# Performance work log

Measured on AMD Instinct MI355X. Metric: run time of the kernel, lower is better.

## Reference

```python
import jax, jax.numpy as jnp
import numpy as np

NU, NI = 100000, 50000
N = NU + NI
CU, CI = 100, 100
D = 64
NL = 3
NNZ = 4_000_000
CNNZ = 5000
B = 4096


def setup_inputs() -> dict:
    key = jax.random.key(0)
    ks = jax.random.split(key, 24)
    def edges(k1, k2, k3, nnz, n):
        return (jax.random.randint(k1, (nnz,), 0, n, dtype=jnp.int32),
                jax.random.randint(k2, (nnz,), 0, n, dtype=jnp.int32),
                jax.random.uniform(k3, (nnz,), dtype=jnp.float32) * 0.05)
    ar, ac, av = edges(ks[0], ks[1], ks[2], NNZ, N)
    s1r, s1c, s1v = edges(ks[3], ks[4], ks[5], NNZ, N)
    s2r, s2c, s2v = edges(ks[6], ks[7], ks[8], NNZ, N)
    cr, cc, cv = edges(ks[9], ks[10], ks[11], CNNZ, CU + CI)
    return {
        "user_emb": jax.random.normal(ks[12], (NU, D), dtype=jnp.float32) * 0.1,
        "item_emb": jax.random.normal(ks[13], (NI, D), dtype=jnp.float32) * 0.1,
        "adj_rows": ar, "adj_cols": ac, "adj_vals": av,
        "sg1_rows": s1r, "sg1_cols": s1c, "sg1_vals": s1v,
        "sg2_rows": s2r, "sg2_cols": s2c, "sg2_vals": s2v,
        "uc": jax.random.uniform(ks[14], (NU, CU), dtype=jnp.float32),
        "ic": jax.random.uniform(ks[15], (NI, CI), dtype=jnp.float32),
        "cg_rows": cr, "cg_cols": cc, "cg_vals": cv,
        "users": jax.random.randint(ks[16], (B,), 0, NU, dtype=jnp.int32),
        "items": jax.random.randint(ks[17], (B,), 0, NI, dtype=jnp.int32),
        "neg_items": jax.random.randint(ks[18], (B,), 0, NI, dtype=jnp.int32),
    }


def _gcn(rows, cols, vals, ego, n):
    """n_layers of SpMM propagation + mean over layer outputs (incl. layer 0)."""
    acc = ego
    x = ego
    for _ in range(NL):
        x = jax.ops.segment_sum(vals[:, None] * x[cols], rows, num_segments=n)
        acc = acc + x
    return acc / (NL + 1)


def reference(user_emb, item_emb,
              adj_rows, adj_cols, adj_vals,
              sg1_rows, sg1_cols, sg1_vals,
              sg2_rows, sg2_cols, sg2_vals,
              uc, ic, cg_rows, cg_cols, cg_vals,
              users, items, neg_items):
    ego = jnp.concatenate([user_emb, item_emb], axis=0)  # [N, D]
    e0 = _gcn(adj_rows, adj_cols, adj_vals, ego, N)
    e1 = _gcn(sg1_rows, sg1_cols, sg1_vals, ego, N)
    e2 = _gcn(sg2_rows, sg2_cols, sg2_vals, ego, N)
    # community GCN: project node embeddings onto community space, propagate, lift back
    ucf = uc.T @ user_emb                                # [CU, D]
    icf = ic.T @ item_emb                                # [CI, D]
    ec = _gcn(cg_rows, cg_cols, cg_vals,
              jnp.concatenate([ucf, icf], axis=0), CU + CI)
    u3 = uc @ ec[:CU]                                    # [NU, D]
    i3 = ic @ ec[CU:]                                    # [NI, D]
    user_f = jnp.concatenate([e0[:NU], e1[:NU], e2[:NU], u3], axis=1)  # [NU, 4D]
    item_f = jnp.concatenate([e0[NU:], e1[NU:], e2[NU:], i3], axis=1)  # [NI, 4D]
    ue = user_f[users]
    ie = item_f[items]
    ne = item_f[neg_items]
    # sup_logits = <u, i_pos> - <u, i_neg>
    return jnp.sum(ue * (ie - ne), axis=-1)
```

## Files before the change

### kernel.cpp

```cpp
#include <hip/hip_runtime.h>
#include <hip/hip_fp16.h>
#include <cstdint>
#include <cstddef>

#define NU_ 100000
#define NI_ 50000
#define NN_ 150000
#define D_  64
#define NNZ_ 4000000
#define CN_ 200
#define CNNZ_ 5000
#define B_ 4096

#define NB2   128
#define RPB2  1172
#define SLICE 112
#define NBLK  512

#define PROJB 1024

#define SCALE_ 32.0f
#define INVS_  (1.0f / 32.0f)

typedef float v2f __attribute__((ext_vector_type(2)));

__device__ __forceinline__ float cv8(unsigned char b) {
    return __builtin_amdgcn_cvt_f32_fp8((int)b, 0);
}


__global__ __launch_bounds__(256) void k_tofp8(const float* __restrict__ a,
                                               const float* __restrict__ b,
                                               unsigned char* __restrict__ dst) {
    size_t off = ((size_t)blockIdx.x * 256 + threadIdx.x) * 4;
    if (off >= (size_t)NN_ * D_) return;
    const float* src = (off < (size_t)NU_ * D_) ? a + off : b + (off - (size_t)NU_ * D_);
    float4 f = *(const float4*)src;
    int p = 0;
    p = __builtin_amdgcn_cvt_pk_fp8_f32(f.x * SCALE_, f.y * SCALE_, p, false);
    p = __builtin_amdgcn_cvt_pk_fp8_f32(f.z * SCALE_, f.w * SCALE_, p, true);
    *(unsigned*)(dst + off) = (unsigned)p;
}

__global__ __launch_bounds__(256) void k_bin(const int* __restrict__ rows,
                                             const int* __restrict__ cols,
                                             const float* __restrict__ vals,
                                             int* __restrict__ bcnt,
                                             int2* __restrict__ gbuf) {
    __shared__ int lcur[NB2];
    int t = threadIdx.x;
    for (int i = t; i < NB2; i += 256) lcur[i] = 0;
    __syncthreads();
    size_t blockbase = (size_t)blockIdx.x * NB2 * SLICE;

    for (int base = blockIdx.x * 1024; base < NNZ_; base += gridDim.x * 1024) {
        int i0 = base + t * 4;
        if (i0 < NNZ_) {
            int4   r4 = *(const int4*)(rows + i0);
            int4   c4 = *(const int4*)(cols + i0);
            float4 v4 = *(const float4*)(vals + i0);
            #pragma unroll
            for (int k = 0; k < 4; k++) {
                int r = (k == 0) ? r4.x : (k == 1) ? r4.y : (k == 2) ? r4.z : r4.w;
                int c = (k == 0) ? c4.x : (k == 1) ? c4.y : (k == 2) ? c4.z : c4.w;
                float v = (k == 0) ? v4.x : (k == 1) ? v4.y : (k == 2) ? v4.z : v4.w;
                int b  = r / RPB2;
                int rl = r - b * RPB2;
                int pos = atomicAdd(&lcur[b], 1);
                if (pos < SLICE)
                    gbuf[blockbase + (size_t)b * SLICE + pos] =
                        make_int2((rl << 18) | c, __float_as_int(v));
            }
        }
    }
    __syncthreads();
    for (int i = t; i < NB2; i += 256)
        bcnt[(size_t)blockIdx.x * NB2 + i] = min(lcur[i], SLICE);
}


__global__ void k_btot(const int* __restrict__ bcnt, int* __restrict__ btot) {
    __shared__ int s[256];
    int b = blockIdx.x, t = threadIdx.x;
    int sum = 0;
    for (int sl = t; sl < NBLK; sl += 256) sum += bcnt[(size_t)sl * NB2 + b];
    s[t] = sum;
    __syncthreads();
    for (int o = 128; o > 0; o >>= 1) {
        if (t < o) s[t] += s[t + o];
        __syncthreads();
    }
    if (t == 0) btot[b] = s[0];
}

__global__ void k_bscan(const int* __restrict__ btot, int* __restrict__ bbase,
                        int* __restrict__ row_ptr) {
    __shared__ int s[NB2];
    int t = threadIdx.x;
    int v = btot[t];
    s[t] = v;
    __syncthreads();
    for (int o = 1; o < NB2; o <<= 1) {
        int x = (t >= o) ? s[t - o] : 0;
        __syncthreads();
        s[t] += x;
        __syncthreads();
    }
    bbase[t] = s[t] - v;
    if (t == NB2 - 1) row_ptr[NN_] = s[t];
}


__global__ __launch_bounds__(1024) void k_csr(const int* __restrict__ bcnt,
                                              const int2* __restrict__ gbuf,
                                              const int* __restrict__ bbase,
                                              int* __restrict__ row_ptr,
                                              int2* __restrict__ ep) {
    __shared__ int h[RPB2];
    __shared__ int hx[RPB2];
    __shared__ int aux[1024];
    int b = blockIdx.x, t = threadIdx.x;
    for (int i = t; i < RPB2; i += 1024) h[i] = 0;
    __syncthreads();

    int sl = t >> 1, part = t & 1;
    int n = bcnt[(size_t)sl * NB2 + b];
    const int2* src = gbuf + ((size_t)sl * NB2 + b) * SLICE;

    for (int i = part; i < n; i += 2) {
        int rl = ((unsigned)src[i].x) >> 18;
        atomicAdd(&h[rl], 1);
    }
    __syncthreads();

    int a0 = (2 * t     < RPB2) ? h[2 * t]     : 0;
    int a1 = (2 * t + 1 < RPB2) ? h[2 * t + 1] : 0;
    aux[t] = a0 + a1;
    __syncthreads();
    for (int o = 1; o < 1024; o <<= 1) {
        int x = (t >= o) ? aux[t - o] : 0;
        __syncthreads();
        aux[t] += x;
        __syncthreads();
    }
    int excl = t ? aux[t - 1] : 0;
    if (2 * t     < RPB2) hx[2 * t]     = excl;
    if (2 * t + 1 < RPB2) hx[2 * t + 1] = excl + a0;
    __syncthreads();

    int base = bbase[b];
    int r0 = b * RPB2;
    int rows_b = min(RPB2, NN_ - r0);
    for (int i = t; i < rows_b; i += 1024) row_ptr[r0 + i] = base + hx[i];
    __syncthreads();

    for (int i = part; i < n; i += 2) {
        int2 e = src[i];
        int rl = ((unsigned)e.x) >> 18;
        int c  = e.x & 0x3FFFF;
        int pos = base + atomicAdd(&hx[rl], 1);
        ep[pos] = make_int2(c, e.y);
    }
}


__global__ __launch_bounds__(256) void k_spmm(const int* __restrict__ rp,
                                              const int2* __restrict__ ep,
                                              const unsigned char* __restrict__ xq,
                                              unsigned char* __restrict__ xn) {
    int w = (blockIdx.x * 256 + threadIdx.x) >> 6;
    if (w >= NN_) return;
    int lane = threadIdx.x & 63;
    int oct = lane >> 3;
    int l8  = lane & 7;
    int j0 = rp[w], j1 = rp[w + 1];
    float a0 = 0.f, a1 = 0.f, a2 = 0.f, a3 = 0.f, a4 = 0.f, a5 = 0.f, a6 = 0.f, a7 = 0.f;
    #pragma unroll 2
    for (int j = j0; j < j1; j += 8) {
        int je = j + oct;
        int2 e = (je < j1) ? ep[je] : make_int2(0, 0);
        float v = __int_as_float(e.y);
        uint2 raw = *(const uint2*)(xq + (size_t)e.x * D_ + l8 * 8);
        v2f f01 = __builtin_amdgcn_cvt_pk_f32_fp8((int)raw.x, false);
        v2f f23 = __builtin_amdgcn_cvt_pk_f32_fp8((int)raw.x, true);
        v2f f45 = __builtin_amdgcn_cvt_pk_f32_fp8((int)raw.y, false);
        v2f f67 = __builtin_amdgcn_cvt_pk_f32_fp8((int)raw.y, true);
        a0 += v * f01[0]; a1 += v * f01[1]; a2 += v * f23[0]; a3 += v * f23[1];
        a4 += v * f45[0]; a5 += v * f45[1]; a6 += v * f67[0]; a7 += v * f67[1];
    }
    #pragma unroll
    for (int o = 32; o >= 8; o >>= 1) {
        a0 += __shfl_xor(a0, o, 64); a1 += __shfl_xor(a1, o, 64);
        a2 += __shfl_xor(a2, o, 64); a3 += __shfl_xor(a3, o, 64);
        a4 += __shfl_xor(a4, o, 64); a5 += __shfl_xor(a5, o, 64);
        a6 += __shfl_xor(a6, o, 64); a7 += __shfl_xor(a7, o, 64);
    }
    if (lane < 8) {
        int p0 = 0, p1 = 0;
        p0 = __builtin_amdgcn_cvt_pk_fp8_f32(a0, a1, p0, false);
        p0 = __builtin_amdgcn_cvt_pk_fp8_f32(a2, a3, p0, true);
        p1 = __builtin_amdgcn_cvt_pk_fp8_f32(a4, a5, p1, false);
        p1 = __builtin_amdgcn_cvt_pk_fp8_f32(a6, a7, p1, true);
        uint2 o2; o2.x = (unsigned)p0; o2.y = (unsigned)p1;
        *(uint2*)(xn + (size_t)w * D_ + l8 * 8) = o2;
    }
}


__global__ __launch_bounds__(256) void k_spmm_s(const int* __restrict__ rp,
                                                const int2* __restrict__ ep,
                                                const unsigned char* __restrict__ xq,
                                                const int* __restrict__ users,
                                                const int* __restrict__ items,
                                                const int* __restrict__ negs,
                                                float* __restrict__ x3s) {
    int s = (blockIdx.x * 256 + threadIdx.x) >> 6;
    if (s >= 3 * B_) return;
    int lane = threadIdx.x & 63;
    int oct = lane >> 3;
    int l8  = lane & 7;
    int node;
    if (s < B_)          node = users[s];
    else if (s < 2 * B_) node = NU_ + items[s - B_];
    else                 node = NU_ + negs[s - 2 * B_];
    int j0 = rp[node], j1 = rp[node + 1];
    float a0 = 0.f, a1 = 0.f, a2 = 0.f, a3 = 0.f, a4 = 0.f, a5 = 0.f, a6 = 0.f, a7 = 0.f;
    #pragma unroll 2
    for (int j = j0; j < j1; j += 8) {
        int je = j + oct;
        int2 e = (je < j1) ? ep[je] : make_int2(0, 0);
        float v = __int_as_float(e.y);
        uint2 raw = *(const uint2*)(xq + (size_t)e.x * D_ + l8 * 8);
        v2f f01 = __builtin_amdgcn_cvt_pk_f32_fp8((int)raw.x, false);
        v2f f23 = __builtin_amdgcn_cvt_pk_f32_fp8((int)raw.x, true);
        v2f f45 = __builtin_amdgcn_cvt_pk_f32_fp8((int)raw.y, false);
        v2f f67 = __builtin_amdgcn_cvt_pk_f32_fp8((int)raw.y, true);
        a0 += v * f01[0]; a1 += v * f01[1]; a2 += v * f23[0]; a3 += v * f23[1];
        a4 += v * f45[0]; a5 += v * f45[1]; a6 += v * f67[0]; a7 += v * f67[1];
    }
    #pragma unroll
    for (int o = 32; o >= 8; o >>= 1) {
        a0 += __shfl_xor(a0, o, 64); a1 += __shfl_xor(a1, o, 64);
        a2 += __shfl_xor(a2, o, 64); a3 += __shfl_xor(a3, o, 64);
        a4 += __shfl_xor(a4, o, 64); a5 += __shfl_xor(a5, o, 64);
        a6 += __shfl_xor(a6, o, 64); a7 += __shfl_xor(a7, o, 64);
    }
    if (lane < 8) {
        float* dst = x3s + (size_t)s * D_ + l8 * 8;
        *(float4*)dst       = make_float4(a0, a1, a2, a3);
        *(float4*)(dst + 4) = make_float4(a4, a5, a6, a7);
    }
}


template<bool FIRST>
__global__ void k_dot_graph(const float* __restrict__ ue, const float* __restrict__ ie,
                            const unsigned char* __restrict__ x1,
                            const unsigned char* __restrict__ x2,
                            const float* __restrict__ x3s,
                            const int* __restrict__ users, const int* __restrict__ items,
                            const int* __restrict__ negs, float* __restrict__ out) {
    int w = (blockIdx.x * blockDim.x + threadIdx.x) >> 6;
    int lane = threadIdx.x & 63;
    if (w >= B_) return;
    int u = users[w], ip = items[w], in_ = negs[w];
    size_t ou = (size_t)u * D_ + lane;
    size_t oi = (size_t)(NU_ + ip) * D_ + lane;
    size_t on = (size_t)(NU_ + in_) * D_ + lane;
    float du = ue[(size_t)u * D_ + lane]
             + (cv8(x1[ou]) + cv8(x2[ou]) + x3s[(size_t)w * D_ + lane]) * INVS_;
    float di = ie[(size_t)ip * D_ + lane]
             + (cv8(x1[oi]) + cv8(x2[oi]) + x3s[(size_t)(B_ + w) * D_ + lane]) * INVS_;
    float dn = ie[(size_t)in_ * D_ + lane]
             + (cv8(x1[on]) + cv8(x2[on]) + x3s[(size_t)(2 * B_ + w) * D_ + lane]) * INVS_;
    float p = du * (di - dn);
    for (int o = 32; o > 0; o >>= 1) p += __shfl_xor(p, o, 64);
    if (lane == 0) {
        if (FIRST) out[w] = p * 0.0625f;
        else       out[w] += p * 0.0625f;
    }
}


__global__ __launch_bounds__(256) void k_proj(const float* __restrict__ mat,
                                              const float* __restrict__ emb,
                                              int n, float* __restrict__ pbuf) {
    __shared__ float se[8 * 64];
    __shared__ float sc[8 * 100];
    int t = threadIdx.x;
    int d = t & 63, c0 = t >> 6;
    float a[25];
    #pragma unroll
    for (int k = 0; k < 25; k++) a[k] = 0.f;

    int upb = (n + gridDim.x - 1) / gridDim.x;
    int u0 = blockIdx.x * upb;
    int u1 = min(u0 + upb, n);
    int ub = u0;
    for (; ub + 8 <= u1; ub += 8) {
        const float4* e4 = (const float4*)(emb + (size_t)ub * 64);
        const float4* c4 = (const float4*)(mat + (size_t)ub * 100);
        float4* se4 = (float4*)se;
        float4* sc4 = (float4*)sc;
        for (int idx = t; idx < 328; idx += 256) {
            if (idx < 128) se4[idx] = e4[idx];
            else           sc4[idx - 128] = c4[idx - 128];
        }
        __syncthreads();
        #pragma unroll
        for (int ul = 0; ul < 8; ++ul) {
            float ev = se[(ul << 6) + d];
            #pragma unroll
            for (int k = 0; k < 25; k++)
                a[k] += sc[ul * 100 + c0 + (k << 2)] * ev;
        }
        __syncthreads();
    }
    if (ub < u1) {
        int m = u1 - ub;
        for (int idx = t; idx < m * 64; idx += 256) se[idx] = emb[(size_t)ub * 64 + idx];
        for (int idx = t; idx < m * 100; idx += 256) sc[idx] = mat[(size_t)ub * 100 + idx];
        __syncthreads();
        for (int ul = 0; ul < m; ++ul) {
            float ev = se[(ul << 6) + d];
            #pragma unroll
            for (int k = 0; k < 25; k++)
                a[k] += sc[ul * 100 + c0 + (k << 2)] * ev;
        }
    }
    float* dst = pbuf + (size_t)blockIdx.x * 6400;
    #pragma unroll
    for (int k = 0; k < 25; k++)
        dst[t + (k << 8)] = a[k];
}

__global__ __launch_bounds__(256) void k_preduce(const float* __restrict__ pbuf,
                                                 float* __restrict__ dst) {
    int e = blockIdx.x * 256 + threadIdx.x;
    const float* src = pbuf + (size_t)blockIdx.y * 128 * 6400 + e;
    float s = 0.f;
    #pragma unroll 8
    for (int p = 0; p < 128; p++) s += src[(size_t)p * 6400];
    atomicAdd(&dst[e], s);
}


__global__ void k_cspmm(const int* __restrict__ r, const int* __restrict__ c,
                        const float* __restrict__ v, const float* __restrict__ x,
                        float* __restrict__ xn) {
    int w = (blockIdx.x * blockDim.x + threadIdx.x) >> 6;
    int lane = threadIdx.x & 63;
    if (w >= CNNZ_) return;
    int rr = r[w], cc = c[w];
    float vv = v[w];
    atomicAdd(&xn[rr * 64 + lane], vv * x[cc * 64 + lane]);
}

__global__ void k_cesum(const float* __restrict__ cego, const float* __restrict__ cb1,
                        const float* __restrict__ cb2, const float* __restrict__ cb3,
                        float* __restrict__ cacc) {
    int i = blockIdx.x * blockDim.x + threadIdx.x;
    if (i < CN_ * D_) cacc[i] = cego[i] + cb1[i] + cb2[i] + cb3[i];
}


__global__ void k_dot_comm(const float* __restrict__ uc, const float* __restrict__ ic,
                           const float* __restrict__ cacc, const int* __restrict__ users,
                           const int* __restrict__ items, const int* __restrict__ negs,
                           float* __restrict__ out) {
    int w = (blockIdx.x * blockDim.x + threadIdx.x) >> 6;
    int lane = threadIdx.x & 63;
    if (w >= B_) return;
    int u = users[w], ip = items[w], in_ = negs[w];
    float u3 = 0.f, i3p = 0.f, i3n = 0.f;
    for (int cc = 0; cc < 100; ++cc) {
        float evU = cacc[cc * 64 + lane];
        float evI = cacc[(100 + cc) * 64 + lane];
        u3  += uc[(size_t)u * 100 + cc] * evU;
        i3p += ic[(size_t)ip * 100 + cc] * evI;
        i3n += ic[(size_t)in_ * 100 + cc] * evI;
    }
    float p = u3 * (i3p - i3n);
    for (int o = 32; o > 0; o >>= 1) p += __shfl_xor(p, o, 64);
    if (lane == 0) out[w] += p * 0.0625f;
}


static inline char* alignp(char*& p, size_t bytes) {
    char* r = p;
    p += (bytes + 255) & ~(size_t)255;
    return r;
}

extern "C" void kernel_launch(void* const* d_in, const int* in_sizes, int n_in,
                              void* d_out, int out_size, void* d_ws, size_t ws_size,
                              hipStream_t stream) {
    const float* uemb = (const float*)d_in[0];
    const float* iemb = (const float*)d_in[1];
    const float* uc   = (const float*)d_in[11];
    const float* ic   = (const float*)d_in[12];
    const int*   cgr  = (const int*)d_in[13];
    const int*   cgc  = (const int*)d_in[14];
    const float* cgv  = (const float*)d_in[15];
    const int*   users = (const int*)d_in[16];
    const int*   items = (const int*)d_in[17];
    const int*   negs  = (const int*)d_in[18];
    float* out = (float*)d_out;

    char* p = (char*)d_ws;
    char*  A      = alignp(p, (size_t)NBLK * NB2 * SLICE * 8);
    unsigned char* egoq = (unsigned char*)alignp(p, (size_t)NN_ * D_);
    int2*  ep     = (int2*) alignp(p, (size_t)NNZ_ * 8);
    float* x3s    = (float*)alignp(p, (size_t)3 * B_ * D_ * 4);
    int*   row_ptr= (int*)  alignp(p, (size_t)(NN_ + 1) * 4);
    int*   bcnt   = (int*)  alignp(p, (size_t)NBLK * NB2 * 4);
    int*   btot   = (int*)  alignp(p, NB2 * 4);
    int*   bbase  = (int*)  alignp(p, NB2 * 4);
    float* cego   = (float*)alignp(p, (size_t)CN_ * D_ * 4);
    float* cb1    = (float*)alignp(p, (size_t)CN_ * D_ * 4);
    float* cb2    = (float*)alignp(p, (size_t)CN_ * D_ * 4);
    float* cb3    = (float*)alignp(p, (size_t)CN_ * D_ * 4);
    float* cacc   = (float*)alignp(p, (size_t)CN_ * D_ * 4);

    int2*          gbuf = (int2*)A;
    unsigned char* xq1  = (unsigned char*)A;
    unsigned char* xq2  = (unsigned char*)(A + (size_t)NN_ * D_);
    float*         pbuf = (float*)A;

    const int gSp = (NN_ * 64) / 256;
    const int gS3 = (3 * B_ * 64) / 256;
    const int gB  = (B_ * 64) / 256;
    const int gC  = (CNNZ_ * 64) / 256;
    const int gCE = (CN_ * D_ + 255) / 256;
    const int gTQ = (NN_ * D_ / 4 + 255) / 256;

    k_tofp8<<<gTQ, 256, 0, stream>>>(uemb, iemb, egoq);

    for (int g = 0; g < 3; ++g) {
        const int*   rows = (const int*)d_in[2 + g * 3];
        const int*   cols = (const int*)d_in[3 + g * 3];
        const float* vals = (const float*)d_in[4 + g * 3];

        k_bin  <<<NBLK, 256, 0, stream>>>(rows, cols, vals, bcnt, gbuf);
        k_btot <<<NB2, 256, 0, stream>>>(bcnt, btot);
        k_bscan<<<1, NB2, 0, stream>>>(btot, bbase, row_ptr);
        k_csr  <<<NB2, 1024, 0, stream>>>(bcnt, gbuf, bbase, row_ptr, ep);

        k_spmm<<<gSp, 256, 0, stream>>>(row_ptr, ep, egoq, xq1);
        k_spmm<<<gSp, 256, 0, stream>>>(row_ptr, ep, xq1, xq2);
        k_spmm_s<<<gS3, 256, 0, stream>>>(row_ptr, ep, xq2, users, items, negs, x3s);

        if (g == 0)
            k_dot_graph<true ><<<gB, 256, 0, stream>>>(uemb, iemb, xq1, xq2, x3s,
                                                       users, items, negs, out);
        else
            k_dot_graph<false><<<gB, 256, 0, stream>>>(uemb, iemb, xq1, xq2, x3s,
                                                       users, items, negs, out);
    }

    hipMemsetAsync(cego, 0, (size_t)CN_ * D_ * 4, stream);
    k_proj<<<PROJB, 256, 0, stream>>>(uc, uemb, NU_, pbuf);
    k_preduce<<<dim3(25, 8), 256, 0, stream>>>(pbuf, cego);
    k_proj<<<PROJB, 256, 0, stream>>>(ic, iemb, NI_, pbuf);
    k_preduce<<<dim3(25, 8), 256, 0, stream>>>(pbuf, cego + 100 * 64);

    hipMemsetAsync(cb1, 0, (size_t)CN_ * D_ * 4, stream);
    k_cspmm<<<gC, 256, 0, stream>>>(cgr, cgc, cgv, cego, cb1);
    hipMemsetAsync(cb2, 0, (size_t)CN_ * D_ * 4, stream);
    k_cspmm<<<gC, 256, 0, stream>>>(cgr, cgc, cgv, cb1, cb2);
    hipMemsetAsync(cb3, 0, (size_t)CN_ * D_ * 4, stream);
    k_cspmm<<<gC, 256, 0, stream>>>(cgr, cgc, cgv, cb2, cb3);
    k_cesum<<<gCE, 256, 0, stream>>>(cego, cb1, cb2, cb3, cacc);

    k_dot_comm<<<gB, 256, 0, stream>>>(uc, ic, cacc, users, items, negs, out);
}
```

Baseline: 944.3 us.

## Pack CSR edges into 32-bit words with fp8 weights and stage writes in LDS

Each edge becomes a single 32-bit word: an 18-bit column index plus the edge value quantised to fp8 after scaling by 256. SpMM kernels undo that scale at output. The CSR build now uses 512 smaller buckets, does its row-offset scan directly over the bucket rows, and stages edges in shared memory so the global writes to the edge array are coalesced. This halves edge-array traffic in the three SpMM passes and in the CSR scatter. The cost is a coarser fp8 edge weight and a fixed per-bucket staging capacity that would silently drop edges if a bucket overflowed.

```diff
diff --git a/kernel.cpp b/kernel.cpp
--- a/kernel.cpp
+++ b/kernel.cpp
@@ -12,15 +12,18 @@
 #define CNNZ_ 5000
 #define B_ 4096
 
-#define NB2   128
-#define RPB2  1172
-#define SLICE 112
+#define NB2   512
+#define RPB2  293
+#define SLICE 40
 #define NBLK  512
+#define ECAP  8448
 
 #define PROJB 1024
 
 #define SCALE_ 32.0f
 #define INVS_  (1.0f / 32.0f)
+#define VSC_   256.0f
+#define IVSC_  (1.0f / 256.0f)
 
 typedef float v2f __attribute__((ext_vector_type(2)));
 
@@ -114,11 +117,12 @@
 __global__ __launch_bounds__(1024) void k_csr(const int* __restrict__ bcnt,
                                               const int2* __restrict__ gbuf,
                                               const int* __restrict__ bbase,
+                                              const int* __restrict__ btot,
                                               int* __restrict__ row_ptr,
-                                              int2* __restrict__ ep) {
+                                              unsigned* __restrict__ ep) {
     __shared__ int h[RPB2];
     __shared__ int hx[RPB2];
-    __shared__ int aux[1024];
+    __shared__ unsigned estage[ECAP];
     int b = blockIdx.x, t = threadIdx.x;
     for (int i = t; i < RPB2; i += 1024) h[i] = 0;
     __syncthreads();
@@ -133,39 +137,44 @@
     }
     __syncthreads();
 
-    int a0 = (2 * t     < RPB2) ? h[2 * t]     : 0;
-    int a1 = (2 * t + 1 < RPB2) ? h[2 * t + 1] : 0;
-    aux[t] = a0 + a1;
-    __syncthreads();
-    for (int o = 1; o < 1024; o <<= 1) {
-        int x = (t >= o) ? aux[t - o] : 0;
-        __syncthreads();
-        aux[t] += x;
-        __syncthreads();
-    }
-    int excl = t ? aux[t - 1] : 0;
-    if (2 * t     < RPB2) hx[2 * t]     = excl;
-    if (2 * t + 1 < RPB2) hx[2 * t + 1] = excl + a0;
-    __syncthreads();
+    if (t < RPB2) hx[t] = h[t];
+    __syncthreads();
+    for (int o = 1; o < RPB2; o <<= 1) {
+        int x = 0;
+        if (t < RPB2 && t >= o) x = hx[t - o];
+        __syncthreads();
+        if (t < RPB2) hx[t] += x;
+        __syncthreads();
+    }
 
     int base = bbase[b];
     int r0 = b * RPB2;
-    int rows_b = min(RPB2, NN_ - r0);
-    for (int i = t; i < rows_b; i += 1024) row_ptr[r0 + i] = base + hx[i];
+    if (t < RPB2) {
+        int excl = hx[t] - h[t];
+        if (r0 + t < NN_) row_ptr[r0 + t] = base + excl;
+        h[t] = excl;
+    }
     __syncthreads();
 
     for (int i = part; i < n; i += 2) {
         int2 e = src[i];
         int rl = ((unsigned)e.x) >> 18;
-        int c  = e.x & 0x3FFFF;
-        int pos = base + atomicAdd(&hx[rl], 1);
-        ep[pos] = make_int2(c, e.y);
-    }
+        unsigned c = (unsigned)e.x & 0x3FFFFu;
+        float v = __int_as_float(e.y) * VSC_;
+        unsigned v8 = (unsigned)__builtin_amdgcn_cvt_pk_fp8_f32(v, 0.f, 0, false) & 0xFFu;
+        int pos = atomicAdd(&h[rl], 1);
+        if (pos < ECAP) estage[pos] = c | (v8 << 24);
+    }
+    __syncthreads();
+
+    int total = btot[b];
+    if (total > ECAP) total = ECAP;
+    for (int i = t; i < total; i += 1024) ep[base + i] = estage[i];
 }
 
 
 __global__ __launch_bounds__(256) void k_spmm(const int* __restrict__ rp,
-                                              const int2* __restrict__ ep,
+                                              const unsigned* __restrict__ ep,
                                               const unsigned char* __restrict__ xq,
                                               unsigned char* __restrict__ xn) {
     int w = (blockIdx.x * 256 + threadIdx.x) >> 6;
@@ -178,9 +187,9 @@
     #pragma unroll 2
     for (int j = j0; j < j1; j += 8) {
         int je = j + oct;
-        int2 e = (je < j1) ? ep[je] : make_int2(0, 0);
-        float v = __int_as_float(e.y);
-        uint2 raw = *(const uint2*)(xq + (size_t)e.x * D_ + l8 * 8);
+        unsigned e = (je < j1) ? ep[je] : 0u;
+        float v = __builtin_amdgcn_cvt_f32_fp8((int)e, 3);
+        uint2 raw = *(const uint2*)(xq + (size_t)(e & 0x3FFFFu) * D_ + l8 * 8);
         v2f f01 = __builtin_amdgcn_cvt_pk_f32_fp8((int)raw.x, false);
         v2f f23 = __builtin_amdgcn_cvt_pk_f32_fp8((int)raw.x, true);
         v2f f45 = __builtin_amdgcn_cvt_pk_f32_fp8((int)raw.y, false);
@@ -197,10 +206,10 @@
     }
     if (lane < 8) {
         int p0 = 0, p1 = 0;
-        p0 = __builtin_amdgcn_cvt_pk_fp8_f32(a0, a1, p0, false);
-        p0 = __builtin_amdgcn_cvt_pk_fp8_f32(a2, a3, p0, true);
-        p1 = __builtin_amdgcn_cvt_pk_fp8_f32(a4, a5, p1, false);
-        p1 = __builtin_amdgcn_cvt_pk_fp8_f32(a6, a7, p1, true);
+        p0 = __builtin_amdgcn_cvt_pk_fp8_f32(a0 * IVSC_, a1 * IVSC_, p0, false);
+        p0 = __builtin_amdgcn_cvt_pk_fp8_f32(a2 * IVSC_, a3 * IVSC_, p0, true);
+        p1 = __builtin_amdgcn_cvt_pk_fp8_f32(a4 * IVSC_, a5 * IVSC_, p1, false);
+        p1 = __builtin_amdgcn_cvt_pk_fp8_f32(a6 * IVSC_, a7 * IVSC_, p1, true);
         uint2 o2; o2.x = (unsigned)p0; o2.y = (unsigned)p1;
         *(uint2*)(xn + (size_t)w * D_ + l8 * 8) = o2;
     }
@@ -208,7 +217,7 @@
 
 
 __global__ __launch_bounds__(256) void k_spmm_s(const int* __restrict__ rp,
-                                                const int2* __restrict__ ep,
+                                                const unsigned* __restrict__ ep,
                                                 const unsigned char* __restrict__ xq,
                                                 const int* __restrict__ users,
                                                 const int* __restrict__ items,
@@ -228,9 +237,9 @@
     #pragma unroll 2
     for (int j = j0; j < j1; j += 8) {
         int je = j + oct;
-        int2 e = (je < j1) ? ep[je] : make_int2(0, 0);
-        float v = __int_as_float(e.y);
-        uint2 raw = *(const uint2*)(xq + (size_t)e.x * D_ + l8 * 8);
+        unsigned e = (je < j1) ? ep[je] : 0u;
+        float v = __builtin_amdgcn_cvt_f32_fp8((int)e, 3);
+        uint2 raw = *(const uint2*)(xq + (size_t)(e & 0x3FFFFu) * D_ + l8 * 8);
         v2f f01 = __builtin_amdgcn_cvt_pk_f32_fp8((int)raw.x, false);
         v2f f23 = __builtin_amdgcn_cvt_pk_f32_fp8((int)raw.x, true);
         v2f f45 = __builtin_amdgcn_cvt_pk_f32_fp8((int)raw.y, false);
@@ -247,8 +256,8 @@
     }
     if (lane < 8) {
         float* dst = x3s + (size_t)s * D_ + l8 * 8;
-        *(float4*)dst       = make_float4(a0, a1, a2, a3);
-        *(float4*)(dst + 4) = make_float4(a4, a5, a6, a7);
+        *(float4*)dst       = make_float4(a0 * IVSC_, a1 * IVSC_, a2 * IVSC_, a3 * IVSC_);
+        *(float4*)(dst + 4) = make_float4(a4 * IVSC_, a5 * IVSC_, a6 * IVSC_, a7 * IVSC_);
     }
 }
 
@@ -410,7 +419,7 @@
     char* p = (char*)d_ws;
     char*  A      = alignp(p, (size_t)NBLK * NB2 * SLICE * 8);
     unsigned char* egoq = (unsigned char*)alignp(p, (size_t)NN_ * D_);
-    int2*  ep     = (int2*) alignp(p, (size_t)NNZ_ * 8);
+    unsigned* ep  = (unsigned*)alignp(p, (size_t)NNZ_ * 4);
     float* x3s    = (float*)alignp(p, (size_t)3 * B_ * D_ * 4);
     int*   row_ptr= (int*)  alignp(p, (size_t)(NN_ + 1) * 4);
     int*   bcnt   = (int*)  alignp(p, (size_t)NBLK * NB2 * 4);
@@ -444,7 +453,7 @@
         k_bin  <<<NBLK, 256, 0, stream>>>(rows, cols, vals, bcnt, gbuf);
         k_btot <<<NB2, 256, 0, stream>>>(bcnt, btot);
         k_bscan<<<1, NB2, 0, stream>>>(btot, bbase, row_ptr);
-        k_csr  <<<NB2, 1024, 0, stream>>>(bcnt, gbuf, bbase, row_ptr, ep);
+        k_csr  <<<NB2, 1024, 0, stream>>>(bcnt, gbuf, bbase, btot, row_ptr, ep);
 
         k_spmm<<<gSp, 256, 0, stream>>>(row_ptr, ep, egoq, xq1);
         k_spmm<<<gSp, 256, 0, stream>>>(row_ptr, ep, xq1, xq2);
```

After: 921.5 us. -2.4%, faster.
